# Performance work log

Hardware: AMD Instinct MI355X
Metric: run time of the kernel (lower is better)

The kernel has to match this reference:

```python
import jax, jax.numpy as jnp
import numpy as np

EPS = 1e-12  # matches torch F.normalize default eps


def setup_inputs() -> dict:
    key = jax.random.key(0)
    ks = jax.random.split(key, 8)
    B, N, D, H = 8, 2048, 128, 128
    s = 1.0 / np.sqrt(D)
    return {
        "x": jax.random.normal(ks[0], (B, N, D), dtype=jnp.float32),
        "edge_weight": jax.random.uniform(ks[1], (B, N, N), dtype=jnp.float32),
        "W0": jax.random.normal(ks[2], (D, H), dtype=jnp.float32) * s,
        "b0": jnp.zeros((H,), dtype=jnp.float32),
        "W1": jax.random.normal(ks[3], (H, H), dtype=jnp.float32) * s,
        "b1": jnp.zeros((H,), dtype=jnp.float32),
        "W2": jax.random.normal(ks[4], (H, H), dtype=jnp.float32) * s,
        "b2": jnp.zeros((H,), dtype=jnp.float32),
    }


def _adapt_conv(h, edge_weight, W, b, is_last):
    h = h @ W + b                                   # [B,N,H]
    norm = jnp.linalg.norm(h, axis=-1, keepdims=True)
    nh = h / jnp.maximum(norm, EPS)                 # L2 normalize (F.normalize)
    cos = jnp.einsum('bij,bkj->bik', nh, nh)        # [B,N,N] cosine similarity
    ew = edge_weight * cos                          # elementwise mask
    h = jnp.einsum('bpq,bqc->bpc', ew, h)           # weighted aggregation
    if not is_last:
        h = jax.nn.relu(h)                          # dropout p=0.0 -> identity
    return h


def reference(x, edge_weight, W0, b0, W1, b1, W2, b2):
    params = [(W0, b0), (W1, b1), (W2, b2)]
    h = x
    n_layers = len(params)
    for i, (W, b) in enumerate(params):
        h = _adapt_conv(h, edge_weight, W, b, is_last=(i == n_layers - 1))
    return h
```

## Files before the change

kernel.cpp:

```cpp
#include <hip/hip_runtime.h>
#include <hip/hip_bf16.h>
#include <math.h>


typedef __attribute__((ext_vector_type(8))) short bf16x8;
typedef __attribute__((ext_vector_type(4))) short bf16x4;
typedef __attribute__((ext_vector_type(4))) float f32x4;

static constexpr int kB = 8, kN = 2048, kH = 128;

static __device__ __forceinline__ ushort bf16bits(float f) {
    __hip_bfloat16 hb = __float2bfloat16(f);
    return *reinterpret_cast<ushort*>(&hb);
}

__global__ __launch_bounds__(256) void cvt_bf16_kernel(
    const float* __restrict__ src, ushort* __restrict__ dst, int n4)
{
    int i = blockIdx.x * 256 + threadIdx.x;
    if (i >= n4) return;
    float4 v = ((const float4*)src)[i];
    bf16x4 o;
    o[0] = (short)bf16bits(v.x); o[1] = (short)bf16bits(v.y);
    o[2] = (short)bf16bits(v.z); o[3] = (short)bf16bits(v.w);
    ((bf16x4*)dst)[i] = o;
}

__global__ __launch_bounds__(256) void cvt_wT_kernel(
    const float* __restrict__ W0, const float* __restrict__ W1,
    const float* __restrict__ W2, ushort* __restrict__ WT)
{
    const float* W = blockIdx.y == 0 ? W0 : (blockIdx.y == 1 ? W1 : W2);
    int i = blockIdx.x * 256 + threadIdx.x;
    int d = i >> 7, c = i & 127;
    WT[(size_t)blockIdx.y * kH * kH + c * kH + d] = bf16bits(W[d * kH + c]);
}

__global__ __launch_bounds__(256) void linear_tr_kernel(
    const ushort* __restrict__ h16, const ushort* __restrict__ WT,
    const float* __restrict__ bias, ushort* __restrict__ t16,
    ushort* __restrict__ tT16, float* __restrict__ invn)
{
    __shared__ float ssb[64][2];
    __shared__ ushort tr[128 * 72];

    const int tid = threadIdx.x, lane = tid & 63, wid = tid >> 6;
    const int wr = wid >> 1, wc = wid & 1, quad = lane >> 4, l16 = lane & 15;
    const int rowbase = blockIdx.x * 64;
    const int b = rowbase / kN, q0 = rowbase % kN;

    f32x4 acc[2][4];
#pragma unroll
    for (int i = 0; i < 2; ++i)
#pragma unroll
        for (int ct = 0; ct < 4; ++ct) acc[i][ct] = (f32x4){0.f, 0.f, 0.f, 0.f};

#pragma unroll
    for (int k = 0; k < 4; ++k) {
        bf16x8 Af[2], Bf[4];
#pragma unroll
        for (int i = 0; i < 2; ++i)
            Af[i] = *(const bf16x8*)&h16[(size_t)(rowbase + wr * 32 + i * 16 + l16) * kH + k * 32 + quad * 8];
#pragma unroll
        for (int ct = 0; ct < 4; ++ct)
            Bf[ct] = *(const bf16x8*)&WT[(size_t)(wc * 64 + ct * 16 + l16) * kH + k * 32 + quad * 8];
#pragma unroll
        for (int i = 0; i < 2; ++i)
#pragma unroll
            for (int ct = 0; ct < 4; ++ct)
                acc[i][ct] = __builtin_amdgcn_mfma_f32_16x16x32_bf16(Af[i], Bf[ct], acc[i][ct], 0, 0, 0);
    }

    float bsr[4];
#pragma unroll
    for (int ct = 0; ct < 4; ++ct) bsr[ct] = bias[wc * 64 + ct * 16 + l16];

    f32x4 ss[2] = {(f32x4){0,0,0,0}, (f32x4){0,0,0,0}};
#pragma unroll
    for (int i = 0; i < 2; ++i)
#pragma unroll
        for (int ct = 0; ct < 4; ++ct)
#pragma unroll
            for (int r = 0; r < 4; ++r) {
                float v = acc[i][ct][r] + bsr[ct];
                acc[i][ct][r] = v;
                ss[i][r] += v * v;
            }
#pragma unroll
    for (int step = 1; step < 16; step <<= 1)
#pragma unroll
        for (int i = 0; i < 2; ++i)
#pragma unroll
            for (int r = 0; r < 4; ++r) ss[i][r] += __shfl_xor(ss[i][r], step);

    if (l16 == 0)
#pragma unroll
        for (int i = 0; i < 2; ++i)
#pragma unroll
            for (int r = 0; r < 4; ++r)
                ssb[wr * 32 + i * 16 + quad * 4 + r][wc] = ss[i][r];
    __syncthreads();
    if (tid < 64) {
        float s2 = ssb[tid][0] + ssb[tid][1];
        invn[rowbase + tid] = 1.f / fmaxf(sqrtf(s2), 1e-12f);
    }

#pragma unroll
    for (int i = 0; i < 2; ++i)
#pragma unroll
        for (int ct = 0; ct < 4; ++ct)
#pragma unroll
            for (int r = 0; r < 4; ++r) {
                const int pl = wr * 32 + i * 16 + quad * 4 + r;
                const int c = wc * 64 + ct * 16 + l16;
                ushort bits = bf16bits(acc[i][ct][r]);
                t16[(size_t)(rowbase + pl) * kH + c] = bits;
                tr[c * 72 + pl] = bits;
            }
    __syncthreads();

    ushort* tTb = tT16 + (size_t)b * kH * kN;
#pragma unroll
    for (int it = 0; it < 4; ++it) {
        int idx = tid + 256 * it;
        int c = idx >> 3, ch = idx & 7;
        bf16x8 v = *(const bf16x8*)&tr[c * 72 + ch * 8];
        *(bf16x8*)&tTb[(size_t)c * kN + q0 + ch * 8] = v;
    }
}

__global__ __launch_bounds__(1024, 4) void agg_kernel(
    const ushort* __restrict__ t, const ushort* __restrict__ tT,
    const float* __restrict__ invn, const float* __restrict__ ew,
    ushort* __restrict__ hout, float* __restrict__ fout, int last)
{
    __shared__ ushort TQ[64 * 136];
    __shared__ ushort TT[128 * 72];
    __shared__ ushort Spm[64 * 72];
    __shared__ float invPs[64];

    const int b = blockIdx.y, pbase = blockIdx.x * 64;
    const int tid = threadIdx.x, lane = tid & 63, wid = tid >> 6;
    const int wp = wid >> 2, wq = wid & 3, quad = lane >> 4, l16 = lane & 15;

    const ushort* tb  = t  + (size_t)b * kN * kH;
    const ushort* tTb = tT + (size_t)b * kH * kN;
    const float*  ewb = ew + (size_t)b * kN * kN;
    const float*  invb = invn + b * kN;

    if (tid < 64) invPs[tid] = invb[pbase + tid];

    bf16x8 Af[4];
#pragma unroll
    for (int k = 0; k < 4; ++k)
        Af[k] = *(const bf16x8*)&tb[(size_t)(pbase + wp * 16 + l16) * kH + k * 32 + quad * 8];

    const int sqRow = tid >> 4, sqCh = tid & 15;
    const int stRow = tid >> 3, stCh = tid & 7;
    bf16x8 rQ = *(const bf16x8*)&tb[(size_t)sqRow * kH + sqCh * 8];
    bf16x8 rT = *(const bf16x8*)&tTb[(size_t)stRow * kN + stCh * 8];

    const int ewRow = pbase + wp * 16 + quad * 4;
    float ewc[4], invQc;
    {
        const int qc = wq * 16 + l16;
        invQc = invb[qc];
#pragma unroll
        for (int r = 0; r < 4; ++r) ewc[r] = ewb[(size_t)(ewRow + r) * kN + qc];
    }

    __syncthreads();
    float invPr[4];
#pragma unroll
    for (int r = 0; r < 4; ++r) invPr[r] = invPs[wp * 16 + quad * 4 + r];

    f32x4 oacc[2] = {(f32x4){0,0,0,0}, (f32x4){0,0,0,0}};

    for (int qt = 0; qt < kN / 64; ++qt) {
        *(bf16x8*)&TQ[sqRow * 136 + sqCh * 8] = rQ;
        *(bf16x8*)&TT[stRow * 72 + stCh * 8]  = rT;
        __syncthreads();

        float ewn[4] = {0.f, 0.f, 0.f, 0.f};
        float invQn = 0.f;
        if (qt + 1 < kN / 64) {
            const int qb2 = (qt + 1) * 64;
            rQ = *(const bf16x8*)&tb[(size_t)(qb2 + sqRow) * kH + sqCh * 8];
            rT = *(const bf16x8*)&tTb[(size_t)stRow * kN + qb2 + stCh * 8];
            const int qc = qb2 + wq * 16 + l16;
            invQn = invb[qc];
#pragma unroll
            for (int r = 0; r < 4; ++r) ewn[r] = ewb[(size_t)(ewRow + r) * kN + qc];
        }

        f32x4 dacc = (f32x4){0.f, 0.f, 0.f, 0.f};
#pragma unroll
        for (int k = 0; k < 4; ++k) {
            bf16x8 Bf = *(const bf16x8*)&TQ[(wq * 16 + l16) * 136 + k * 32 + quad * 8];
            dacc = __builtin_amdgcn_mfma_f32_16x16x32_bf16(Af[k], Bf, dacc, 0, 0, 0);
        }
#pragma unroll
        for (int r = 0; r < 4; ++r)
            Spm[(wp * 16 + quad * 4 + r) * 72 + wq * 16 + l16] = bf16bits(dacc[r] * ewc[r] * invQc);
        __syncthreads();

#pragma unroll
        for (int k = 0; k < 2; ++k) {
            bf16x8 Sa = *(const bf16x8*)&Spm[(wp * 16 + l16) * 72 + k * 32 + quad * 8];
#pragma unroll
            for (int ct = 0; ct < 2; ++ct) {
                bf16x8 Bb = *(const bf16x8*)&TT[(wq * 32 + ct * 16 + l16) * 72 + k * 32 + quad * 8];
                oacc[ct] = __builtin_amdgcn_mfma_f32_16x16x32_bf16(Sa, Bb, oacc[ct], 0, 0, 0);
            }
        }
        __syncthreads();

#pragma unroll
        for (int r = 0; r < 4; ++r) ewc[r] = ewn[r];
        invQc = invQn;
    }

#pragma unroll
    for (int ct = 0; ct < 2; ++ct)
#pragma unroll
        for (int r = 0; r < 4; ++r) {
            const int p = pbase + wp * 16 + quad * 4 + r;
            const int c = wq * 32 + ct * 16 + l16;
            float v = oacc[ct][r] * invPr[r];
            if (!last) {
                hout[(size_t)b * kN * kH + (size_t)p * kH + c] = bf16bits(fmaxf(v, 0.f));
            } else {
                fout[(size_t)b * kN * kH + (size_t)p * kH + c] = v;
            }
        }
}

extern "C" void kernel_launch(void* const* d_in, const int* in_sizes, int n_in,
                              void* d_out, int out_size, void* d_ws, size_t ws_size,
                              hipStream_t stream) {
    const float* x  = (const float*)d_in[0];
    const float* ew = (const float*)d_in[1];
    const float* W0 = (const float*)d_in[2];
    const float* b0 = (const float*)d_in[3];
    const float* W1 = (const float*)d_in[4];
    const float* b1 = (const float*)d_in[5];
    const float* W2 = (const float*)d_in[6];
    const float* b2 = (const float*)d_in[7];
    const float* bias[3] = {b0, b1, b2};

    const size_t nBNH = (size_t)kB * kN * kH;
    ushort* h16  = (ushort*)d_ws;
    ushort* t16  = h16 + nBNH;
    ushort* tT16 = t16 + nBNH;
    float*  invn = (float*)(tT16 + nBNH);
    ushort* WT   = (ushort*)(invn + (size_t)kB * kN);
    float*  out  = (float*)d_out;

    cvt_bf16_kernel<<<(int)(nBNH / 4 + 255) / 256, 256, 0, stream>>>(x, h16, (int)(nBNH / 4));
    cvt_wT_kernel<<<dim3(64, 3), 256, 0, stream>>>(W0, W1, W2, WT);

    for (int layer = 0; layer < 3; ++layer) {
        linear_tr_kernel<<<kB * kN / 64, 256, 0, stream>>>(
            h16, WT + (size_t)layer * kH * kH, bias[layer], t16, tT16, invn);
        agg_kernel<<<dim3(kN / 64, kB), 1024, 0, stream>>>(
            t16, tT16, invn, ew, h16, out, layer == 2 ? 1 : 0);
    }
}
```

Baseline: 341.2 us.

## Halve agg block to 512 threads with larger per-wave tiles and split-K reduction

Rewrites the aggregation kernel to use 8 waves instead of 16. Each wave now computes 32 rows of the similarity tile and a 32x64 output sub-tile, splitting the inner K of 64 between wave pairs. The partial sums are reduced through shared memory aliased over the staging buffers at the end. The aim is more MFMA work per LDS fragment load and fewer waves synchronising at each barrier, at the cost of more registers, fewer threads to hide memory latency, and an extra reduction pass.

```diff
diff --git a/kernel.cpp b/kernel.cpp
--- a/kernel.cpp
+++ b/kernel.cpp
@@ -129,19 +129,23 @@
     }
 }
 
-__global__ __launch_bounds__(1024, 4) void agg_kernel(
+__global__ __launch_bounds__(512, 4) void agg_kernel(
     const ushort* __restrict__ t, const ushort* __restrict__ tT,
     const float* __restrict__ invn, const float* __restrict__ ew,
     ushort* __restrict__ hout, float* __restrict__ fout, int last)
 {
-    __shared__ ushort TQ[64 * 136];
-    __shared__ ushort TT[128 * 72];
-    __shared__ ushort Spm[64 * 72];
-    __shared__ float invPs[64];
+    __shared__ char smem[45312];
+    ushort* TQ   = (ushort*)smem;
+    ushort* TT   = (ushort*)(smem + 17408);
+    ushort* Spm  = (ushort*)(smem + 35840);
+    float* invPs = (float*)(smem + 45056);
+    float* redbuf = (float*)smem;
 
     const int b = blockIdx.y, pbase = blockIdx.x * 64;
     const int tid = threadIdx.x, lane = tid & 63, wid = tid >> 6;
-    const int wp = wid >> 2, wq = wid & 3, quad = lane >> 4, l16 = lane & 15;
+    const int quad = lane >> 4, l16 = lane & 15;
+    const int wsp = wid >> 2, wsq = wid & 3;
+    const int wop = wid >> 2, woc = (wid >> 1) & 1, wok = wid & 1;
 
     const ushort* tb  = t  + (size_t)b * kN * kH;
     const ushort* tTb = tT + (size_t)b * kH * kN;
@@ -150,89 +154,127 @@
 
     if (tid < 64) invPs[tid] = invb[pbase + tid];
 
-    bf16x8 Af[4];
-#pragma unroll
-    for (int k = 0; k < 4; ++k)
-        Af[k] = *(const bf16x8*)&tb[(size_t)(pbase + wp * 16 + l16) * kH + k * 32 + quad * 8];
-
-    const int sqRow = tid >> 4, sqCh = tid & 15;
-    const int stRow = tid >> 3, stCh = tid & 7;
-    bf16x8 rQ = *(const bf16x8*)&tb[(size_t)sqRow * kH + sqCh * 8];
-    bf16x8 rT = *(const bf16x8*)&tTb[(size_t)stRow * kN + stCh * 8];
-
-    const int ewRow = pbase + wp * 16 + quad * 4;
-    float ewc[4], invQc;
-    {
-        const int qc = wq * 16 + l16;
-        invQc = invb[qc];
-#pragma unroll
-        for (int r = 0; r < 4; ++r) ewc[r] = ewb[(size_t)(ewRow + r) * kN + qc];
-    }
+    bf16x8 Af[2][4];
+#pragma unroll
+    for (int it = 0; it < 2; ++it)
+#pragma unroll
+        for (int k = 0; k < 4; ++k)
+            Af[it][k] = *(const bf16x8*)&tb[(size_t)(pbase + wsp * 32 + it * 16 + l16) * kH + k * 32 + quad * 8];
+
+    const int qrow = tid >> 3, qoff = (tid & 7) * 16;
+    const int trow = tid >> 2, toff = (tid & 3) * 16;
+
+    bf16x8 rQ0 = *(const bf16x8*)&tb[(size_t)qrow * kH + qoff];
+    bf16x8 rQ1 = *(const bf16x8*)&tb[(size_t)qrow * kH + qoff + 8];
+    bf16x8 rT0 = *(const bf16x8*)&tTb[(size_t)trow * kN + toff];
+    bf16x8 rT1 = *(const bf16x8*)&tTb[(size_t)trow * kN + toff + 8];
+
+    const int ewq = wsq * 16 + l16;
+    float ewc[2][4], invQc = invb[ewq];
+#pragma unroll
+    for (int it = 0; it < 2; ++it)
+#pragma unroll
+        for (int r = 0; r < 4; ++r)
+            ewc[it][r] = ewb[(size_t)(pbase + wsp * 32 + it * 16 + quad * 4 + r) * kN + ewq];
+
+    f32x4 oacc[2][4];
+#pragma unroll
+    for (int it = 0; it < 2; ++it)
+#pragma unroll
+        for (int ct = 0; ct < 4; ++ct) oacc[it][ct] = (f32x4){0.f, 0.f, 0.f, 0.f};
 
     __syncthreads();
-    float invPr[4];
-#pragma unroll
-    for (int r = 0; r < 4; ++r) invPr[r] = invPs[wp * 16 + quad * 4 + r];
-
-    f32x4 oacc[2] = {(f32x4){0,0,0,0}, (f32x4){0,0,0,0}};
 
     for (int qt = 0; qt < kN / 64; ++qt) {
-        *(bf16x8*)&TQ[sqRow * 136 + sqCh * 8] = rQ;
-        *(bf16x8*)&TT[stRow * 72 + stCh * 8]  = rT;
+        const int qbase = qt * 64;
+
+        *(bf16x8*)&TQ[qrow * 136 + qoff]     = rQ0;
+        *(bf16x8*)&TQ[qrow * 136 + qoff + 8] = rQ1;
+        *(bf16x8*)&TT[trow * 72 + toff]      = rT0;
+        *(bf16x8*)&TT[trow * 72 + toff + 8]  = rT1;
         __syncthreads();
 
-        float ewn[4] = {0.f, 0.f, 0.f, 0.f};
+        float ewn[2][4] = {{0,0,0,0},{0,0,0,0}};
         float invQn = 0.f;
         if (qt + 1 < kN / 64) {
-            const int qb2 = (qt + 1) * 64;
-            rQ = *(const bf16x8*)&tb[(size_t)(qb2 + sqRow) * kH + sqCh * 8];
-            rT = *(const bf16x8*)&tTb[(size_t)stRow * kN + qb2 + stCh * 8];
-            const int qc = qb2 + wq * 16 + l16;
-            invQn = invb[qc];
-#pragma unroll
-            for (int r = 0; r < 4; ++r) ewn[r] = ewb[(size_t)(ewRow + r) * kN + qc];
+            const int qb2 = qbase + 64;
+            rQ0 = *(const bf16x8*)&tb[(size_t)(qb2 + qrow) * kH + qoff];
+            rQ1 = *(const bf16x8*)&tb[(size_t)(qb2 + qrow) * kH + qoff + 8];
+            rT0 = *(const bf16x8*)&tTb[(size_t)trow * kN + qb2 + toff];
+            rT1 = *(const bf16x8*)&tTb[(size_t)trow * kN + qb2 + toff + 8];
+            invQn = invb[qb2 + ewq];
+#pragma unroll
+            for (int it = 0; it < 2; ++it)
+#pragma unroll
+                for (int r = 0; r < 4; ++r)
+                    ewn[it][r] = ewb[(size_t)(pbase + wsp * 32 + it * 16 + quad * 4 + r) * kN + qb2 + ewq];
         }
 
-        f32x4 dacc = (f32x4){0.f, 0.f, 0.f, 0.f};
+        f32x4 dacc[2] = {(f32x4){0,0,0,0}, (f32x4){0,0,0,0}};
 #pragma unroll
         for (int k = 0; k < 4; ++k) {
-            bf16x8 Bf = *(const bf16x8*)&TQ[(wq * 16 + l16) * 136 + k * 32 + quad * 8];
-            dacc = __builtin_amdgcn_mfma_f32_16x16x32_bf16(Af[k], Bf, dacc, 0, 0, 0);
+            bf16x8 Bf = *(const bf16x8*)&TQ[(wsq * 16 + l16) * 136 + k * 32 + quad * 8];
+            dacc[0] = __builtin_amdgcn_mfma_f32_16x16x32_bf16(Af[0][k], Bf, dacc[0], 0, 0, 0);
+            dacc[1] = __builtin_amdgcn_mfma_f32_16x16x32_bf16(Af[1][k], Bf, dacc[1], 0, 0, 0);
         }
 #pragma unroll
-        for (int r = 0; r < 4; ++r)
-            Spm[(wp * 16 + quad * 4 + r) * 72 + wq * 16 + l16] = bf16bits(dacc[r] * ewc[r] * invQc);
+        for (int it = 0; it < 2; ++it)
+#pragma unroll
+            for (int r = 0; r < 4; ++r)
+                Spm[(wsp * 32 + it * 16 + quad * 4 + r) * 72 + wsq * 16 + l16] =
+                    bf16bits(dacc[it][r] * ewc[it][r] * invQc);
         __syncthreads();
 
-#pragma unroll
-        for (int k = 0; k < 2; ++k) {
-            bf16x8 Sa = *(const bf16x8*)&Spm[(wp * 16 + l16) * 72 + k * 32 + quad * 8];
-#pragma unroll
-            for (int ct = 0; ct < 2; ++ct) {
-                bf16x8 Bb = *(const bf16x8*)&TT[(wq * 32 + ct * 16 + l16) * 72 + k * 32 + quad * 8];
-                oacc[ct] = __builtin_amdgcn_mfma_f32_16x16x32_bf16(Sa, Bb, oacc[ct], 0, 0, 0);
-            }
+        bf16x8 Sa[2];
+#pragma unroll
+        for (int it = 0; it < 2; ++it)
+            Sa[it] = *(const bf16x8*)&Spm[(wop * 32 + it * 16 + l16) * 72 + wok * 32 + quad * 8];
+#pragma unroll
+        for (int ct = 0; ct < 4; ++ct) {
+            bf16x8 Bb = *(const bf16x8*)&TT[(woc * 64 + ct * 16 + l16) * 72 + wok * 32 + quad * 8];
+            oacc[0][ct] = __builtin_amdgcn_mfma_f32_16x16x32_bf16(Sa[0], Bb, oacc[0][ct], 0, 0, 0);
+            oacc[1][ct] = __builtin_amdgcn_mfma_f32_16x16x32_bf16(Sa[1], Bb, oacc[1][ct], 0, 0, 0);
         }
         __syncthreads();
 
 #pragma unroll
-        for (int r = 0; r < 4; ++r) ewc[r] = ewn[r];
-        invQc = invQn;
-    }
-
-#pragma unroll
-    for (int ct = 0; ct < 2; ++ct)
-#pragma unroll
-        for (int r = 0; r < 4; ++r) {
-            const int p = pbase + wp * 16 + quad * 4 + r;
-            const int c = wq * 32 + ct * 16 + l16;
-            float v = oacc[ct][r] * invPr[r];
-            if (!last) {
-                hout[(size_t)b * kN * kH + (size_t)p * kH + c] = bf16bits(fmaxf(v, 0.f));
-            } else {
-                fout[(size_t)b * kN * kH + (size_t)p * kH + c] = v;
-            }
+        for (int it = 0; it < 2; ++it) {
+            invQc = invQn;
+#pragma unroll
+            for (int r = 0; r < 4; ++r) ewc[it][r] = ewn[it][r];
         }
+    }
+
+    if (wok == 1) {
+        float* rb = redbuf + (wop * 2 + woc) * 2080;
+#pragma unroll
+        for (int it = 0; it < 2; ++it)
+#pragma unroll
+            for (int ct = 0; ct < 4; ++ct)
+#pragma unroll
+                for (int r = 0; r < 4; ++r)
+                    rb[(it * 16 + quad * 4 + r) * 65 + ct * 16 + l16] = oacc[it][ct][r];
+    }
+    __syncthreads();
+    if (wok == 0) {
+        float* rb = redbuf + (wop * 2 + woc) * 2080;
+#pragma unroll
+        for (int it = 0; it < 2; ++it)
+#pragma unroll
+            for (int ct = 0; ct < 4; ++ct)
+#pragma unroll
+                for (int r = 0; r < 4; ++r) {
+                    const int pl = wop * 32 + it * 16 + quad * 4 + r;
+                    const int p = pbase + pl;
+                    const int c = woc * 64 + ct * 16 + l16;
+                    float v = (oacc[it][ct][r] + rb[(it * 16 + quad * 4 + r) * 65 + ct * 16 + l16]) * invPs[pl];
+                    if (!last) {
+                        hout[(size_t)b * kN * kH + (size_t)p * kH + c] = bf16bits(fmaxf(v, 0.f));
+                    } else {
+                        fout[(size_t)b * kN * kH + (size_t)p * kH + c] = v;
+                    }
+                }
+    }
 }
 
 extern "C" void kernel_launch(void* const* d_in, const int* in_sizes, int n_in,
@@ -262,7 +304,7 @@
     for (int layer = 0; layer < 3; ++layer) {
         linear_tr_kernel<<<kB * kN / 64, 256, 0, stream>>>(
             h16, WT + (size_t)layer * kH * kH, bias[layer], t16, tT16, invn);
-        agg_kernel<<<dim3(kN / 64, kB), 1024, 0, stream>>>(
+        agg_kernel<<<dim3(kN / 64, kB), 512, 0, stream>>>(
             t16, tT16, invn, ew, h16, out, layer == 2 ? 1 : 0);
     }
 }
```

Result: slower. 350.9 us (+2.8%).

## Pre-convert edge weights to fp16 and retile aggregation to 32-row blocks

Applied to the files above, without the earlier changes.

Adds a one-time kernel that converts the fp32 edge_weight matrix to fp16 in workspace, so each of the three aggregation layers reads 2-byte instead of 4-byte weights. The aggregation kernel is retiled from 1024-thread, 64-row blocks to 256-thread, 32-row blocks with 2 blocks per CU; each wave now computes two similarity tiles and four output tiles. The intent is to cut edge-weight bandwidth and improve per-wave MFMA reuse. In exchange it adds an extra full pass over the edge matrix and doubles the number of blocks that restream the t and tT tiles. It also adds fp16 rounding of the edge weights and requires more workspace.

```diff
diff --git a/kernel.cpp b/kernel.cpp
--- a/kernel.cpp
+++ b/kernel.cpp
@@ -1,5 +1,6 @@
 #include <hip/hip_runtime.h>
 #include <hip/hip_bf16.h>
+#include <hip/hip_fp16.h>
 #include <math.h>
 
 
@@ -12,6 +13,14 @@
 static __device__ __forceinline__ ushort bf16bits(float f) {
     __hip_bfloat16 hb = __float2bfloat16(f);
     return *reinterpret_cast<ushort*>(&hb);
+}
+static __device__ __forceinline__ ushort f16bits(float f) {
+    __half h = __float2half(f);
+    return *reinterpret_cast<ushort*>(&h);
+}
+static __device__ __forceinline__ float f16val(ushort u) {
+    __half h = *reinterpret_cast<__half*>(&u);
+    return __half2float(h);
 }
 
 __global__ __launch_bounds__(256) void cvt_bf16_kernel(
@@ -26,6 +35,17 @@
     ((bf16x4*)dst)[i] = o;
 }
 
+__global__ __launch_bounds__(256) void cvt_ew_kernel(
+    const float* __restrict__ ew, ushort* __restrict__ ew16)
+{
+    int i = blockIdx.x * 256 + threadIdx.x;
+    float4 v = ((const float4*)ew)[i];
+    bf16x4 o;
+    o[0] = (short)f16bits(v.x); o[1] = (short)f16bits(v.y);
+    o[2] = (short)f16bits(v.z); o[3] = (short)f16bits(v.w);
+    ((bf16x4*)ew16)[i] = o;
+}
+
 __global__ __launch_bounds__(256) void cvt_wT_kernel(
     const float* __restrict__ W0, const float* __restrict__ W1,
     const float* __restrict__ W2, ushort* __restrict__ WT)
@@ -129,104 +149,130 @@
     }
 }
 
-__global__ __launch_bounds__(1024, 4) void agg_kernel(
+__global__ __launch_bounds__(256, 2) void agg_kernel(
     const ushort* __restrict__ t, const ushort* __restrict__ tT,
-    const float* __restrict__ invn, const float* __restrict__ ew,
+    const float* __restrict__ invn, const ushort* __restrict__ ew16,
     ushort* __restrict__ hout, float* __restrict__ fout, int last)
 {
     __shared__ ushort TQ[64 * 136];
     __shared__ ushort TT[128 * 72];
-    __shared__ ushort Spm[64 * 72];
-    __shared__ float invPs[64];
-
-    const int b = blockIdx.y, pbase = blockIdx.x * 64;
+    __shared__ ushort Spm[32 * 72];
+    __shared__ float invPs[32];
+
+    const int b = blockIdx.y, pbase = blockIdx.x * 32;
     const int tid = threadIdx.x, lane = tid & 63, wid = tid >> 6;
-    const int wp = wid >> 2, wq = wid & 3, quad = lane >> 4, l16 = lane & 15;
+    const int quad = lane >> 4, l16 = lane & 15;
+    const int wsp = wid >> 1, wsq = wid & 1;
+    const int wop = wid >> 1, woc = wid & 1;
 
     const ushort* tb  = t  + (size_t)b * kN * kH;
     const ushort* tTb = tT + (size_t)b * kH * kN;
-    const float*  ewb = ew + (size_t)b * kN * kN;
+    const ushort* ewb = ew16 + (size_t)b * kN * kN;
     const float*  invb = invn + b * kN;
 
-    if (tid < 64) invPs[tid] = invb[pbase + tid];
+    if (tid < 32) invPs[tid] = invb[pbase + tid];
 
     bf16x8 Af[4];
 #pragma unroll
     for (int k = 0; k < 4; ++k)
-        Af[k] = *(const bf16x8*)&tb[(size_t)(pbase + wp * 16 + l16) * kH + k * 32 + quad * 8];
-
-    const int sqRow = tid >> 4, sqCh = tid & 15;
-    const int stRow = tid >> 3, stCh = tid & 7;
-    bf16x8 rQ = *(const bf16x8*)&tb[(size_t)sqRow * kH + sqCh * 8];
-    bf16x8 rT = *(const bf16x8*)&tTb[(size_t)stRow * kN + stCh * 8];
-
-    const int ewRow = pbase + wp * 16 + quad * 4;
-    float ewc[4], invQc;
-    {
-        const int qc = wq * 16 + l16;
-        invQc = invb[qc];
-#pragma unroll
-        for (int r = 0; r < 4; ++r) ewc[r] = ewb[(size_t)(ewRow + r) * kN + qc];
-    }
+        Af[k] = *(const bf16x8*)&tb[(size_t)(pbase + wsp * 16 + l16) * kH + k * 32 + quad * 8];
+
+    const int qrow = tid >> 2, qcol = (tid & 3) * 8;
+    const int trow = tid >> 3, tcol = (tid & 7) * 8;
+
+    bf16x8 rQ[4], rT[4];
+#pragma unroll
+    for (int j = 0; j < 4; ++j) {
+        rQ[j] = *(const bf16x8*)&tb[(size_t)qrow * kH + qcol + j * 32];
+        rT[j] = *(const bf16x8*)&tTb[(size_t)(trow + j * 32) * kN + tcol];
+    }
+
+    const int ewRow = pbase + wsp * 16 + quad * 4;
+    ushort ewc[2][4], ewn[2][4];
+    float invQc[2], invQn[2];
+#pragma unroll
+    for (int jt = 0; jt < 2; ++jt) {
+        const int qc = wsq * 32 + jt * 16 + l16;
+        invQc[jt] = invb[qc];
+#pragma unroll
+        for (int r = 0; r < 4; ++r) ewc[jt][r] = ewb[(size_t)(ewRow + r) * kN + qc];
+    }
+
+    f32x4 oacc[4];
+#pragma unroll
+    for (int ct = 0; ct < 4; ++ct) oacc[ct] = (f32x4){0.f, 0.f, 0.f, 0.f};
 
     __syncthreads();
-    float invPr[4];
-#pragma unroll
-    for (int r = 0; r < 4; ++r) invPr[r] = invPs[wp * 16 + quad * 4 + r];
-
-    f32x4 oacc[2] = {(f32x4){0,0,0,0}, (f32x4){0,0,0,0}};
 
     for (int qt = 0; qt < kN / 64; ++qt) {
-        *(bf16x8*)&TQ[sqRow * 136 + sqCh * 8] = rQ;
-        *(bf16x8*)&TT[stRow * 72 + stCh * 8]  = rT;
+        const int qbase = qt * 64;
+
+#pragma unroll
+        for (int j = 0; j < 4; ++j) {
+            *(bf16x8*)&TQ[qrow * 136 + qcol + j * 32] = rQ[j];
+            *(bf16x8*)&TT[(trow + j * 32) * 72 + tcol] = rT[j];
+        }
         __syncthreads();
 
-        float ewn[4] = {0.f, 0.f, 0.f, 0.f};
-        float invQn = 0.f;
         if (qt + 1 < kN / 64) {
-            const int qb2 = (qt + 1) * 64;
-            rQ = *(const bf16x8*)&tb[(size_t)(qb2 + sqRow) * kH + sqCh * 8];
-            rT = *(const bf16x8*)&tTb[(size_t)stRow * kN + qb2 + stCh * 8];
-            const int qc = qb2 + wq * 16 + l16;
-            invQn = invb[qc];
-#pragma unroll
-            for (int r = 0; r < 4; ++r) ewn[r] = ewb[(size_t)(ewRow + r) * kN + qc];
-        }
-
-        f32x4 dacc = (f32x4){0.f, 0.f, 0.f, 0.f};
+            const int qb2 = qbase + 64;
+#pragma unroll
+            for (int j = 0; j < 4; ++j) {
+                rQ[j] = *(const bf16x8*)&tb[(size_t)(qb2 + qrow) * kH + qcol + j * 32];
+                rT[j] = *(const bf16x8*)&tTb[(size_t)(trow + j * 32) * kN + qb2 + tcol];
+            }
+#pragma unroll
+            for (int jt = 0; jt < 2; ++jt) {
+                const int qc = qb2 + wsq * 32 + jt * 16 + l16;
+                invQn[jt] = invb[qc];
+#pragma unroll
+                for (int r = 0; r < 4; ++r) ewn[jt][r] = ewb[(size_t)(ewRow + r) * kN + qc];
+            }
+        }
+
+        f32x4 dacc[2] = {(f32x4){0,0,0,0}, (f32x4){0,0,0,0}};
 #pragma unroll
         for (int k = 0; k < 4; ++k) {
-            bf16x8 Bf = *(const bf16x8*)&TQ[(wq * 16 + l16) * 136 + k * 32 + quad * 8];
-            dacc = __builtin_amdgcn_mfma_f32_16x16x32_bf16(Af[k], Bf, dacc, 0, 0, 0);
-        }
-#pragma unroll
-        for (int r = 0; r < 4; ++r)
-            Spm[(wp * 16 + quad * 4 + r) * 72 + wq * 16 + l16] = bf16bits(dacc[r] * ewc[r] * invQc);
+            bf16x8 Bf0 = *(const bf16x8*)&TQ[(wsq * 32 + l16) * 136 + k * 32 + quad * 8];
+            bf16x8 Bf1 = *(const bf16x8*)&TQ[(wsq * 32 + 16 + l16) * 136 + k * 32 + quad * 8];
+            dacc[0] = __builtin_amdgcn_mfma_f32_16x16x32_bf16(Af[k], Bf0, dacc[0], 0, 0, 0);
+            dacc[1] = __builtin_amdgcn_mfma_f32_16x16x32_bf16(Af[k], Bf1, dacc[1], 0, 0, 0);
+        }
+#pragma unroll
+        for (int jt = 0; jt < 2; ++jt)
+#pragma unroll
+            for (int r = 0; r < 4; ++r)
+                Spm[(wsp * 16 + quad * 4 + r) * 72 + wsq * 32 + jt * 16 + l16] =
+                    bf16bits(dacc[jt][r] * f16val(ewc[jt][r]) * invQc[jt]);
         __syncthreads();
 
 #pragma unroll
-        for (int k = 0; k < 2; ++k) {
-            bf16x8 Sa = *(const bf16x8*)&Spm[(wp * 16 + l16) * 72 + k * 32 + quad * 8];
-#pragma unroll
-            for (int ct = 0; ct < 2; ++ct) {
-                bf16x8 Bb = *(const bf16x8*)&TT[(wq * 32 + ct * 16 + l16) * 72 + k * 32 + quad * 8];
+        for (int k2 = 0; k2 < 2; ++k2) {
+            bf16x8 Sa = *(const bf16x8*)&Spm[(wop * 16 + l16) * 72 + k2 * 32 + quad * 8];
+#pragma unroll
+            for (int ct = 0; ct < 4; ++ct) {
+                bf16x8 Bb = *(const bf16x8*)&TT[(woc * 64 + ct * 16 + l16) * 72 + k2 * 32 + quad * 8];
                 oacc[ct] = __builtin_amdgcn_mfma_f32_16x16x32_bf16(Sa, Bb, oacc[ct], 0, 0, 0);
             }
         }
         __syncthreads();
 
 #pragma unroll
-        for (int r = 0; r < 4; ++r) ewc[r] = ewn[r];
-        invQc = invQn;
-    }
-
-#pragma unroll
-    for (int ct = 0; ct < 2; ++ct)
+        for (int jt = 0; jt < 2; ++jt) {
+            invQc[jt] = invQn[jt];
+#pragma unroll
+            for (int r = 0; r < 4; ++r) ewc[jt][r] = ewn[jt][r];
+        }
+    }
+
+#pragma unroll
+    for (int ct = 0; ct < 4; ++ct)
 #pragma unroll
         for (int r = 0; r < 4; ++r) {
-            const int p = pbase + wp * 16 + quad * 4 + r;
-            const int c = wq * 32 + ct * 16 + l16;
-            float v = oacc[ct][r] * invPr[r];
+            const int pl = wop * 16 + quad * 4 + r;
+            const int p = pbase + pl;
+            const int c = woc * 64 + ct * 16 + l16;
+            float v = oacc[ct][r] * invPs[pl];
             if (!last) {
                 hout[(size_t)b * kN * kH + (size_t)p * kH + c] = bf16bits(fmaxf(v, 0.f));
             } else {
@@ -249,20 +295,23 @@
     const float* bias[3] = {b0, b1, b2};
 
     const size_t nBNH = (size_t)kB * kN * kH;
+    const size_t nBNN = (size_t)kB * kN * kN;
     ushort* h16  = (ushort*)d_ws;
     ushort* t16  = h16 + nBNH;
     ushort* tT16 = t16 + nBNH;
     float*  invn = (float*)(tT16 + nBNH);
     ushort* WT   = (ushort*)(invn + (size_t)kB * kN);
+    ushort* ew16 = WT + (size_t)3 * kH * kH;
     float*  out  = (float*)d_out;
 
+    cvt_ew_kernel<<<(int)(nBNN / 4 / 256), 256, 0, stream>>>(ew, ew16);
     cvt_bf16_kernel<<<(int)(nBNH / 4 + 255) / 256, 256, 0, stream>>>(x, h16, (int)(nBNH / 4));
     cvt_wT_kernel<<<dim3(64, 3), 256, 0, stream>>>(W0, W1, W2, WT);
 
     for (int layer = 0; layer < 3; ++layer) {
         linear_tr_kernel<<<kB * kN / 64, 256, 0, stream>>>(
             h16, WT + (size_t)layer * kH * kH, bias[layer], t16, tT16, invn);
-        agg_kernel<<<dim3(kN / 64, kB), 1024, 0, stream>>>(
-            t16, tT16, invn, ew, h16, out, layer == 2 ? 1 : 0);
-    }
-}
+        agg_kernel<<<dim3(kN / 32, kB), 256, 0, stream>>>(
+            t16, tT16, invn, ew16, h16, out, layer == 2 ? 1 : 0);
+    }
+}
```

Measured after the change: 387.1 us. 1.13x slower.
